# Kernel tuning notes

Hardware: AMD Instinct MI355X
Metric: run time of the kernel (lower is better)

Reference implementation:

```python
import jax, jax.numpy as jnp
import numpy as np

B, N, K, C_IN, M, C_OUT = 2, 20000, 16, 128, 9, 128


def setup_inputs() -> dict:
    key = jax.random.key(0)
    k1, k2, k3, k4, k5, k6 = jax.random.split(key, 6)
    x = jax.random.normal(k1, (B, N, C_IN), dtype=jnp.float32)
    # 0 == "no neighbor" (maps to the prepended zero row); valid ids are 1..N
    adj = jax.random.randint(k2, (N, K), 0, N, dtype=jnp.int32)
    W = jax.random.uniform(k3, (M, C_OUT, C_IN), jnp.float32, -0.05, 0.05)
    b = jax.random.uniform(k4, (C_OUT,), jnp.float32, -0.05, 0.05)
    u = jax.random.uniform(k5, (M, C_IN), jnp.float32, -0.05, 0.05)
    c = jax.random.uniform(k6, (M,), jnp.float32, -0.05, 0.05)
    return {"x": x, "adj": adj, "W": W, "b": b, "u": u, "c": c}


def reference(x, adj, W, b, u, c):
    Bb, Nn, Cin = x.shape
    # prepend zero row so adj==0 gathers zeros (padding neighbor)
    xp = jnp.concatenate([jnp.zeros((Bb, 1, Cin), x.dtype), x], axis=1)
    patches = xp[:, adj]                      # [B, N, K, C] neighbor features
    # pseudo-coordinate differences -> soft assignment over M kernels
    diff = x[:, :, None, :] - patches          # [B, N, K, C]
    logits = jnp.einsum('bnkc,mc->bnkm', diff, u) + c
    q = jax.nn.softmax(logits, axis=-1)        # softmax over M (last axis)
    # inverse neighbor count (0 where the node has no neighbors)
    deg = jnp.count_nonzero(adj, axis=1).astype(x.dtype)        # [N]
    deg_inv = jnp.where(deg > 0, 1.0 / jnp.maximum(deg, 1.0), 0.0)
    # out[b,n,o] = deg_inv[n] * sum_{k,m} q[b,n,k,m] * (W[m] @ x_nbr)[o]
    msg = jnp.einsum('bnkm,moc,bnkc->bno', q, W, patches)        # [B, N, O]
    return msg * deg_inv[None, :, None] + b
```

## Files before the change

### kernel.cpp

```cpp
#include <hip/hip_runtime.h>
#include <hip/hip_bf16.h>

#define NB 2
#define NN 20000
#define NKN 16
#define NC 128
#define NM 9
#define NO 128
#define NR (NB*NN)
#define KK 1152
#define NPB 32
#define YS 12
#define YB (NR/64)
#define SROW 2304
#define PBASE 73728u
#define SMEMB 139264

typedef short bf16x8 __attribute__((ext_vector_type(8)));
typedef short bf16x4 __attribute__((ext_vector_type(4)));
typedef float f32x4  __attribute__((ext_vector_type(4)));
typedef unsigned short u16x8 __attribute__((ext_vector_type(8)));

typedef __attribute__((address_space(1))) const void gas_void;
typedef __attribute__((address_space(3))) void las_void;

union frg8 { bf16x4 h[2]; bf16x8 v; };

__device__ inline unsigned short bfb(float f) {
    union { __hip_bfloat16 b; unsigned short u; } t;
    t.b = __float2bfloat16(f);
    return t.u;
}

__global__ __launch_bounds__(256) void prep_kernel(const float* __restrict__ x,
                                                   const float* __restrict__ u,
                                                   const float* __restrict__ W,
                                                   float* __restrict__ y,
                                                   __hip_bfloat16* __restrict__ xb,
                                                   __hip_bfloat16* __restrict__ Wg,
                                                   int use_xb) {
    int tid = threadIdx.x;
    if (blockIdx.x < YB) {
        int wave = tid >> 6, lane = tid & 63;
        int lr = lane & 15, quad = lane >> 4;
        int node0 = blockIdx.x * 64 + wave * 16;
        long xbase = (long)(node0 + lr) * NC;

        bf16x8 afr[4];
        #pragma unroll
        for (int kc = 0; kc < 4; kc++) {
            const float* px = x + xbase + kc * 32 + quad * 8;
            float4 a0 = *(const float4*)px;
            float4 a1 = *(const float4*)(px + 4);
            union { bf16x8 v; unsigned short s[8]; __hip_bfloat16 h[8]; } af;
            af.h[0] = __float2bfloat16(a0.x); af.h[1] = __float2bfloat16(a0.y);
            af.h[2] = __float2bfloat16(a0.z); af.h[3] = __float2bfloat16(a0.w);
            af.h[4] = __float2bfloat16(a1.x); af.h[5] = __float2bfloat16(a1.y);
            af.h[6] = __float2bfloat16(a1.z); af.h[7] = __float2bfloat16(a1.w);
            afr[kc] = af.v;
            if (use_xb)
                *(u16x8*)((unsigned short*)xb + xbase + kc * 32 + quad * 8) =
                    *(u16x8*)&af.v;
        }
        int cs = (lr < NM) ? lr : 0;
        float fz = (lr < NM) ? 1.f : 0.f;
        f32x4 acc = (f32x4){0.f, 0.f, 0.f, 0.f};
        #pragma unroll
        for (int kc = 0; kc < 4; kc++) {
            const float* pu = u + cs * NC + kc * 32 + quad * 8;
            float4 b0 = *(const float4*)pu;
            float4 b1 = *(const float4*)(pu + 4);
            union { bf16x8 v; __hip_bfloat16 h[8]; } bf;
            bf.h[0] = __float2bfloat16(b0.x * fz); bf.h[1] = __float2bfloat16(b0.y * fz);
            bf.h[2] = __float2bfloat16(b0.z * fz); bf.h[3] = __float2bfloat16(b0.w * fz);
            bf.h[4] = __float2bfloat16(b1.x * fz); bf.h[5] = __float2bfloat16(b1.y * fz);
            bf.h[6] = __float2bfloat16(b1.z * fz); bf.h[7] = __float2bfloat16(b1.w * fz);
            acc = __builtin_amdgcn_mfma_f32_16x16x32_bf16(afr[kc], bf.v, acc, 0, 0, 0);
        }
        if (lr < NM) {
            #pragma unroll
            for (int r = 0; r < 4; r++)
                y[(long)(node0 + quad * 4 + r) * YS + lr] = acc[r];
        }
    } else {
        int t = (blockIdx.x - YB) * 256 + tid;
        int kk = t >> 7;
        int o = t & 127;
        int ctt = kk / 144;
        int rem = kk - ctt * 144;
        int m = rem >> 4;
        int ci = rem & 15;
        float v = W[m * 16384 + o * 128 + ctt * 16 + ci];
        Wg[((kk >> 5) * 128 + o) * 32 + (kk & 31)] = __float2bfloat16(v);
    }
}

template<bool BF16G>
__global__ __launch_bounds__(1024, 4) void fused_kernel(const float* __restrict__ x,
                                                        const __hip_bfloat16* __restrict__ xb,
                                                        const int* __restrict__ adj,
                                                        const float* __restrict__ y,
                                                        const float* __restrict__ cv,
                                                        const __hip_bfloat16* __restrict__ Wg,
                                                        const float* __restrict__ bv,
                                                        float* __restrict__ out) {
    __shared__ __align__(16) char smem[SMEMB];

    int tid = threadIdx.x;
    int lane = tid & 63, wv = tid >> 6;
    int lr = lane & 15, quad = lane >> 4;
    int node0 = blockIdx.x * NPB;
    int b = node0 / NN;
    int n0 = node0 - b * NN;

    bool sm = (lane < 32);
    int lnode = wv * 2 + (quad & 1);
    int a = 0;
    if (sm) a = adj[(n0 + lnode) * NKN + lr];
    int rowint = b * NN + ((a > 0) ? a - 1 : 0);

    float4 yn0 = {0,0,0,0}, yn1 = {0,0,0,0}, ya0 = {0,0,0,0}, ya1 = {0,0,0,0};
    float yn8 = 0.f, ya8 = 0.f;
    if (sm) {
        const float* yn = y + (long)(node0 + lnode) * YS;
        const float* ya = y + (long)rowint * YS;
        yn0 = *(const float4*)yn;  yn1 = *(const float4*)(yn + 4);  yn8 = yn[8];
        ya0 = *(const float4*)ya;  ya1 = *(const float4*)(ya + 4);  ya8 = ya[8];
    }

    unsigned long long mk = __ballot(a > 0);
    int d = (int)__popcll((mk >> (quad * 16)) & 0xFFFFull);
    float di = (d > 0) ? 1.f / (float)d : 0.f;

    int pos = lane & 31;
    int e   = ((pos >> 3) << 2) | ((pos >> 1) & 3);
    int hh  = pos & 1;
    int ctl = lane >> 5;
    int rowA = __shfl(rowint, e);
    int rowB = __shfl(rowint, 16 + e);

    unsigned wboff = PBASE + (unsigned)(wv * 4096);
    unsigned sb = (unsigned)(uintptr_t)&smem[0];
    unsigned wba = sb + wboff;

    if (sm) {
        float sel = (a > 0) ? 1.f : 0.f;
        float l[NM];
        l[0] = yn0.x - sel * ya0.x + cv[0];
        l[1] = yn0.y - sel * ya0.y + cv[1];
        l[2] = yn0.z - sel * ya0.z + cv[2];
        l[3] = yn0.w - sel * ya0.w + cv[3];
        l[4] = yn1.x - sel * ya1.x + cv[4];
        l[5] = yn1.y - sel * ya1.y + cv[5];
        l[6] = yn1.z - sel * ya1.z + cv[6];
        l[7] = yn1.w - sel * ya1.w + cv[7];
        l[8] = yn8   - sel * ya8   + cv[8];
        float mx = l[0];
        #pragma unroll
        for (int m = 1; m < NM; m++) mx = fmaxf(mx, l[m]);
        float e_[NM]; float sum = 0.f;
        #pragma unroll
        for (int m = 0; m < NM; m++) { e_[m] = expf(l[m] - mx); sum += e_[m]; }
        float qf = ((a > 0) ? (1.f / sum) : 0.f) * di;

        union { u16x8 v[2]; unsigned short s[16]; } H, L;
        #pragma unroll
        for (int m = 0; m < NM; m++) {
            float qv = e_[m] * qf;
            unsigned short hb = bfb(qv);
            union { unsigned short u; __hip_bfloat16 bb; } hv; hv.u = hb;
            H.s[m] = hb;
            L.s[m] = bfb(qv - __bfloat162float(hv.bb));
        }
        #pragma unroll
        for (int m = NM; m < 16; m++) { H.s[m] = 0; L.s[m] = 0; }

        unsigned qo = wboff + (unsigned)((quad & 1) * 1024 +
                                         (lr >> 2) * 128 + (lr & 3) * 32);
        *(u16x8*)(smem + qo)       = H.v[0];
        *(u16x8*)(smem + qo + 16)  = H.v[1];
        *(u16x8*)(smem + qo + 512) = L.v[0];
        *(u16x8*)(smem + qo + 528) = L.v[1];
    }
    asm volatile("s_waitcnt lgkmcnt(0)" ::: "memory");
    __builtin_amdgcn_sched_barrier(0);

    bf16x4 qa0, qa1, qb0, qb1;
    unsigned qra = wba + (unsigned)(quad * 256 + lr * 8);
    asm volatile("ds_read_b64_tr_b16 %0, %2 offset:0\n\t"
                 "ds_read_b64_tr_b16 %1, %2 offset:128"
                 : "=&v"(qa0), "=&v"(qa1) : "v"(qra));
    asm volatile("ds_read_b64_tr_b16 %0, %2 offset:1024\n\t"
                 "ds_read_b64_tr_b16 %1, %2 offset:1152"
                 : "=&v"(qb0), "=&v"(qb1) : "v"(qra));
    asm volatile("s_waitcnt lgkmcnt(0)" ::: "memory");
    __builtin_amdgcn_sched_barrier(0);
    frg8 fragA, fragB;
    fragA.h[0] = qa0; fragA.h[1] = qa1;
    fragB.h[0] = qb0; fragB.h[1] = qb1;

    #define ISSUE(S) {                                                          \
        long rr = (long)(((S) >> 2) ? rowB : rowA);                             \
        const __hip_bfloat16* gp = xb + rr * NC +                               \
                                   (2 * ((S) & 3) + ctl) * 16 + hh * 8;         \
        __builtin_amdgcn_global_load_lds((gas_void*)gp,                         \
            (las_void*)(smem + wboff + (unsigned)(((S) & 3) * 1024)), 16, 0, 0);\
    }

    #define PITER(S, NW) {                                                      \
        if (BF16G) {                                                            \
            asm volatile("s_waitcnt vmcnt(" #NW ")" ::: "memory");              \
            __builtin_amdgcn_sched_barrier(0);                                  \
        } else {                                                                \
            long rr_ = (long)(((S) >> 2) ? rowB : rowA);                        \
            const float* fp = x + rr_ * NC + (2 * ((S) & 3) + ctl) * 16 + hh * 8;\
            float4 f0 = *(const float4*)fp;                                     \
            float4 f1 = *(const float4*)(fp + 4);                               \
            union { u16x8 v; unsigned short s[8]; } ov;                         \
            ov.s[0] = bfb(f0.x); ov.s[1] = bfb(f0.y); ov.s[2] = bfb(f0.z);      \
            ov.s[3] = bfb(f0.w); ov.s[4] = bfb(f1.x); ov.s[5] = bfb(f1.y);      \
            ov.s[6] = bfb(f1.z); ov.s[7] = bfb(f1.w);                           \
            *(u16x8*)(smem + wboff + (unsigned)(((S) & 3) * 1024 + lane * 16))  \
                = ov.v;                                                         \
            asm volatile("s_waitcnt lgkmcnt(0)" ::: "memory");                  \
            __builtin_amdgcn_sched_barrier(0);                                  \
        }                                                                       \
        bf16x4 p0a, p0b, p1a, p1b;                                              \
        unsigned pr_ = wba + (unsigned)(((S) & 3) * 1024 +                      \
                                        (quad & 1) * 256 + lr * 8);             \
        asm volatile("ds_read_b64_tr_b16 %0, %4 offset:0\n\t"                   \
                     "ds_read_b64_tr_b16 %1, %4 offset:128\n\t"                 \
                     "ds_read_b64_tr_b16 %2, %4 offset:512\n\t"                 \
                     "ds_read_b64_tr_b16 %3, %4 offset:640"                     \
                     : "=&v"(p0a), "=&v"(p0b), "=&v"(p1a), "=&v"(p1b)           \
                     : "v"(pr_));                                               \
        asm volatile("s_waitcnt lgkmcnt(0)" ::: "memory");                      \
        __builtin_amdgcn_sched_barrier(0);                                      \
        if (BF16G && (S) < 4) { ISSUE((S) + 4) }                                \
        {                                                                       \
            int nl_ = 2 * wv + ((S) >> 2);                                      \
            unsigned swz_ = (unsigned)((nl_ & 7) << 4);                         \
            f32x4 z = (f32x4){0.f, 0.f, 0.f, 0.f};                              \
            frg8 pf; pf.h[0] = p0a; pf.h[1] = p0b;                              \
            f32x4 ac = __builtin_amdgcn_mfma_f32_16x16x32_bf16(pf.v,            \
                           ((S) >> 2) ? fragB.v : fragA.v, z, 0, 0, 0);         \
            bf16x4 sv;                                                          \
            sv[0] = (short)bfb(ac[0]); sv[1] = (short)bfb(ac[1]);               \
            sv[2] = (short)bfb(ac[2]); sv[3] = (short)bfb(ac[3]);               \
            unsigned so = ((unsigned)((2 * ((S) & 3)) * 288 + lr * 32 +         \
                                      quad * 8)) ^ swz_;                        \
            if (lr < 9) *(bf16x4*)(smem + nl_ * SROW + so) = sv;                \
            pf.h[0] = p1a; pf.h[1] = p1b;                                       \
            ac = __builtin_amdgcn_mfma_f32_16x16x32_bf16(pf.v,                  \
                     ((S) >> 2) ? fragB.v : fragA.v, z, 0, 0, 0);               \
            sv[0] = (short)bfb(ac[0]); sv[1] = (short)bfb(ac[1]);               \
            sv[2] = (short)bfb(ac[2]); sv[3] = (short)bfb(ac[3]);               \
            so = ((unsigned)((2 * ((S) & 3) + 1) * 288 + lr * 32 +              \
                             quad * 8)) ^ swz_;                                 \
            if (lr < 9) *(bf16x4*)(smem + nl_ * SROW + so) = sv;                \
        }                                                                       \
    }

    if (BF16G) {
        asm volatile("s_waitcnt vmcnt(0)" ::: "memory");
        __builtin_amdgcn_sched_barrier(0);
        ISSUE(0) ISSUE(1) ISSUE(2) ISSUE(3)
    }
    PITER(0, 3) PITER(1, 3) PITER(2, 3) PITER(3, 3)
    PITER(4, 3) PITER(5, 2) PITER(6, 1) PITER(7, 0)
    #undef PITER
    #undef ISSUE

    __syncthreads();
    __builtin_amdgcn_sched_barrier(0);

    if (wv < 8) {
        const short* wg = reinterpret_cast<const short*>(Wg);
        f32x4 acc0 = (f32x4){0.f, 0.f, 0.f, 0.f};
        f32x4 acc1 = (f32x4){0.f, 0.f, 0.f, 0.f};
        unsigned swzB = (unsigned)((lr & 7) << 4);
        #pragma unroll 9
        for (int kc = 0; kc < 36; kc++) {
            bf16x8 bfrag = *(const bf16x8*)(wg + ((kc * 128) + wv * 16 + lr) * 32
                                            + quad * 8);
            unsigned ao = ((unsigned)(kc * 64 + quad * 16)) ^ swzB;
            bf16x8 a0 = *(const bf16x8*)(smem + (unsigned)(lr * SROW) + ao);
            bf16x8 a1 = *(const bf16x8*)(smem + (unsigned)((16 + lr) * SROW) + ao);
            acc0 = __builtin_amdgcn_mfma_f32_16x16x32_bf16(a0, bfrag, acc0, 0, 0, 0);
            acc1 = __builtin_amdgcn_mfma_f32_16x16x32_bf16(a1, bfrag, acc1, 0, 0, 0);
        }

        int col = wv * 16 + lr;
        float bb = bv[col];
        int rbase = node0 + quad * 4;
        #pragma unroll
        for (int r = 0; r < 4; r++) {
            out[(long)(rbase + r) * NO + col]      = acc0[r] + bb;
            out[(long)(rbase + 16 + r) * NO + col] = acc1[r] + bb;
        }
    }
}

extern "C" void kernel_launch(void* const* d_in, const int* in_sizes, int n_in,
                              void* d_out, int out_size, void* d_ws, size_t ws_size,
                              hipStream_t stream) {
    const float* x   = (const float*)d_in[0];
    const int*   adj = (const int*)  d_in[1];
    const float* W   = (const float*)d_in[2];
    const float* bv  = (const float*)d_in[3];
    const float* u   = (const float*)d_in[4];
    const float* cv  = (const float*)d_in[5];
    float* out = (float*)d_out;

    char* ws = (char*)d_ws;
    float* y = (float*)ws;
    __hip_bfloat16* Wg = (__hip_bfloat16*)(ws + 1920000);
    __hip_bfloat16* xb = (__hip_bfloat16*)(ws + 2214912);
    bool use_xb = (ws_size >= (size_t)12454912);

    prep_kernel<<<YB + 576, 256, 0, stream>>>(x, u, W, y, use_xb ? xb : nullptr, Wg,
                                              use_xb ? 1 : 0);
    if (use_xb)
        fused_kernel<true><<<NR / NPB, 1024, 0, stream>>>(x, xb, adj, y, cv, Wg, bv, out);
    else
        fused_kernel<false><<<NR / NPB, 1024, 0, stream>>>(x, xb, adj, y, cv, Wg, bv, out);
}
```

Measured before the change: 139.4 us.

## Halve nodes per block and software-pipeline LDS transpose reads across gather stages

Cuts the block to 16 nodes and 512 threads, halving shared memory so more blocks fit per CU, and every wave now joins the final GEMM with one accumulator instead of half the waves idling. The gather loop is restructured so the transposed LDS reads for the next slot are issued before the MFMA and store of the current slot, using double-buffered fragments and finer lgkmcnt/vmcnt waits. This aims to hide LDS and global latency and raise occupancy. In exchange, each Wg fragment is now loaded by twice as many blocks, and the hand-tuned wait counts risk ordering mistakes.

```diff
diff --git a/kernel.cpp b/kernel.cpp
--- a/kernel.cpp
+++ b/kernel.cpp
@@ -9,12 +9,12 @@
 #define NO 128
 #define NR (NB*NN)
 #define KK 1152
-#define NPB 32
+#define NPB 16
 #define YS 12
 #define YB (NR/64)
 #define SROW 2304
-#define PBASE 73728u
-#define SMEMB 139264
+#define PBASE 36864u
+#define SMEMB 69632
 
 typedef short bf16x8 __attribute__((ext_vector_type(8)));
 typedef short bf16x4 __attribute__((ext_vector_type(4)));
@@ -96,14 +96,14 @@
 }
 
 template<bool BF16G>
-__global__ __launch_bounds__(1024, 4) void fused_kernel(const float* __restrict__ x,
-                                                        const __hip_bfloat16* __restrict__ xb,
-                                                        const int* __restrict__ adj,
-                                                        const float* __restrict__ y,
-                                                        const float* __restrict__ cv,
-                                                        const __hip_bfloat16* __restrict__ Wg,
-                                                        const float* __restrict__ bv,
-                                                        float* __restrict__ out) {
+__global__ __launch_bounds__(512, 4) void fused_kernel(const float* __restrict__ x,
+                                                       const __hip_bfloat16* __restrict__ xb,
+                                                       const int* __restrict__ adj,
+                                                       const float* __restrict__ y,
+                                                       const float* __restrict__ cv,
+                                                       const __hip_bfloat16* __restrict__ Wg,
+                                                       const float* __restrict__ bv,
+                                                       float* __restrict__ out) {
     __shared__ __align__(16) char smem[SMEMB];
 
     int tid = threadIdx.x;
@@ -207,77 +207,101 @@
             (las_void*)(smem + wboff + (unsigned)(((S) & 3) * 1024)), 16, 0, 0);\
     }
 
-    #define PITER(S, NW) {                                                      \
-        if (BF16G) {                                                            \
-            asm volatile("s_waitcnt vmcnt(" #NW ")" ::: "memory");              \
-            __builtin_amdgcn_sched_barrier(0);                                  \
-        } else {                                                                \
-            long rr_ = (long)(((S) >> 2) ? rowB : rowA);                        \
-            const float* fp = x + rr_ * NC + (2 * ((S) & 3) + ctl) * 16 + hh * 8;\
-            float4 f0 = *(const float4*)fp;                                     \
-            float4 f1 = *(const float4*)(fp + 4);                               \
-            union { u16x8 v; unsigned short s[8]; } ov;                         \
-            ov.s[0] = bfb(f0.x); ov.s[1] = bfb(f0.y); ov.s[2] = bfb(f0.z);      \
-            ov.s[3] = bfb(f0.w); ov.s[4] = bfb(f1.x); ov.s[5] = bfb(f1.y);      \
-            ov.s[6] = bfb(f1.z); ov.s[7] = bfb(f1.w);                           \
-            *(u16x8*)(smem + wboff + (unsigned)(((S) & 3) * 1024 + lane * 16))  \
-                = ov.v;                                                         \
-            asm volatile("s_waitcnt lgkmcnt(0)" ::: "memory");                  \
-            __builtin_amdgcn_sched_barrier(0);                                  \
-        }                                                                       \
-        bf16x4 p0a, p0b, p1a, p1b;                                              \
-        unsigned pr_ = wba + (unsigned)(((S) & 3) * 1024 +                      \
-                                        (quad & 1) * 256 + lr * 8);             \
+    #define TRREAD(D0, D1, D2, D3, SLOT) {                                      \
+        unsigned pr_ = wba + (unsigned)((SLOT) * 1024 + (quad & 1) * 256 +      \
+                                        lr * 8);                                \
         asm volatile("ds_read_b64_tr_b16 %0, %4 offset:0\n\t"                   \
                      "ds_read_b64_tr_b16 %1, %4 offset:128\n\t"                 \
                      "ds_read_b64_tr_b16 %2, %4 offset:512\n\t"                 \
                      "ds_read_b64_tr_b16 %3, %4 offset:640"                     \
-                     : "=&v"(p0a), "=&v"(p0b), "=&v"(p1a), "=&v"(p1b)           \
+                     : "=&v"(D0), "=&v"(D1), "=&v"(D2), "=&v"(D3)               \
                      : "v"(pr_));                                               \
-        asm volatile("s_waitcnt lgkmcnt(0)" ::: "memory");                      \
-        __builtin_amdgcn_sched_barrier(0);                                      \
-        if (BF16G && (S) < 4) { ISSUE((S) + 4) }                                \
-        {                                                                       \
-            int nl_ = 2 * wv + ((S) >> 2);                                      \
-            unsigned swz_ = (unsigned)((nl_ & 7) << 4);                         \
-            f32x4 z = (f32x4){0.f, 0.f, 0.f, 0.f};                              \
-            frg8 pf; pf.h[0] = p0a; pf.h[1] = p0b;                              \
-            f32x4 ac = __builtin_amdgcn_mfma_f32_16x16x32_bf16(pf.v,            \
-                           ((S) >> 2) ? fragB.v : fragA.v, z, 0, 0, 0);         \
-            bf16x4 sv;                                                          \
-            sv[0] = (short)bfb(ac[0]); sv[1] = (short)bfb(ac[1]);               \
-            sv[2] = (short)bfb(ac[2]); sv[3] = (short)bfb(ac[3]);               \
-            unsigned so = ((unsigned)((2 * ((S) & 3)) * 288 + lr * 32 +         \
-                                      quad * 8)) ^ swz_;                        \
-            if (lr < 9) *(bf16x4*)(smem + nl_ * SROW + so) = sv;                \
-            pf.h[0] = p1a; pf.h[1] = p1b;                                       \
-            ac = __builtin_amdgcn_mfma_f32_16x16x32_bf16(pf.v,                  \
-                     ((S) >> 2) ? fragB.v : fragA.v, z, 0, 0, 0);               \
-            sv[0] = (short)bfb(ac[0]); sv[1] = (short)bfb(ac[1]);               \
-            sv[2] = (short)bfb(ac[2]); sv[3] = (short)bfb(ac[3]);               \
-            so = ((unsigned)((2 * ((S) & 3) + 1) * 288 + lr * 32 +              \
-                             quad * 8)) ^ swz_;                                 \
-            if (lr < 9) *(bf16x4*)(smem + nl_ * SROW + so) = sv;                \
-        }                                                                       \
+    }
+
+    #define MFMA_STORE(S, F0, F1, F2, F3) {                                     \
+        int nl_ = 2 * wv + ((S) >> 2);                                          \
+        unsigned swz_ = (unsigned)((nl_ & 7) << 4);                             \
+        f32x4 z = (f32x4){0.f, 0.f, 0.f, 0.f};                                  \
+        frg8 pf; pf.h[0] = F0; pf.h[1] = F1;                                    \
+        f32x4 ac = __builtin_amdgcn_mfma_f32_16x16x32_bf16(pf.v,                \
+                       ((S) >> 2) ? fragB.v : fragA.v, z, 0, 0, 0);             \
+        bf16x4 sv;                                                              \
+        sv[0] = (short)bfb(ac[0]); sv[1] = (short)bfb(ac[1]);                   \
+        sv[2] = (short)bfb(ac[2]); sv[3] = (short)bfb(ac[3]);                   \
+        unsigned so = ((unsigned)((2 * ((S) & 3)) * 288 + lr * 32 +             \
+                                  quad * 8)) ^ swz_;                            \
+        if (lr < 9) *(bf16x4*)(smem + nl_ * SROW + so) = sv;                    \
+        pf.h[0] = F2; pf.h[1] = F3;                                             \
+        ac = __builtin_amdgcn_mfma_f32_16x16x32_bf16(pf.v,                      \
+                 ((S) >> 2) ? fragB.v : fragA.v, z, 0, 0, 0);                   \
+        sv[0] = (short)bfb(ac[0]); sv[1] = (short)bfb(ac[1]);                   \
+        sv[2] = (short)bfb(ac[2]); sv[3] = (short)bfb(ac[3]);                   \
+        so = ((unsigned)((2 * ((S) & 3) + 1) * 288 + lr * 32 +                  \
+                         quad * 8)) ^ swz_;                                     \
+        if (lr < 9) *(bf16x4*)(smem + nl_ * SROW + so) = sv;                    \
     }
 
     if (BF16G) {
+        #define ITER(S, LKS, VWS, C0, C1, C2, C3, N0, N1, N2, N3, DOV) {        \
+            asm volatile("s_waitcnt lgkmcnt(" LKS ")" ::: "memory");            \
+            __builtin_amdgcn_sched_barrier(0);                                  \
+            if ((S) < 4) { ISSUE((S) + 4) }                                     \
+            if (DOV) {                                                          \
+                asm volatile("s_waitcnt vmcnt(" VWS ")" ::: "memory");          \
+                __builtin_amdgcn_sched_barrier(0);                              \
+                TRREAD(N0, N1, N2, N3, ((S) + 1) & 3)                           \
+            }                                                                   \
+            MFMA_STORE(S, C0, C1, C2, C3)                                       \
+        }
+
         asm volatile("s_waitcnt vmcnt(0)" ::: "memory");
         __builtin_amdgcn_sched_barrier(0);
         ISSUE(0) ISSUE(1) ISSUE(2) ISSUE(3)
-    }
-    PITER(0, 3) PITER(1, 3) PITER(2, 3) PITER(3, 3)
-    PITER(4, 3) PITER(5, 2) PITER(6, 1) PITER(7, 0)
-    #undef PITER
+        asm volatile("s_waitcnt vmcnt(3)" ::: "memory");
+        __builtin_amdgcn_sched_barrier(0);
+        bf16x4 cf0, cf1, cf2, cf3, nf0, nf1, nf2, nf3;
+        TRREAD(cf0, cf1, cf2, cf3, 0)
+
+        ITER(0, "0", "3", cf0, cf1, cf2, cf3, nf0, nf1, nf2, nf3, 1)
+        ITER(1, "2", "3", nf0, nf1, nf2, nf3, cf0, cf1, cf2, cf3, 1)
+        ITER(2, "2", "3", cf0, cf1, cf2, cf3, nf0, nf1, nf2, nf3, 1)
+        ITER(3, "2", "3", nf0, nf1, nf2, nf3, cf0, cf1, cf2, cf3, 1)
+        ITER(4, "2", "2", cf0, cf1, cf2, cf3, nf0, nf1, nf2, nf3, 1)
+        ITER(5, "2", "1", nf0, nf1, nf2, nf3, cf0, cf1, cf2, cf3, 1)
+        ITER(6, "2", "0", cf0, cf1, cf2, cf3, nf0, nf1, nf2, nf3, 1)
+        ITER(7, "2", "0", nf0, nf1, nf2, nf3, cf0, cf1, cf2, cf3, 0)
+        #undef ITER
+    } else {
+        #pragma unroll
+        for (int S = 0; S < 8; ++S) {
+            long rr_ = (long)((S >= 4) ? rowB : rowA);
+            const float* fp = x + rr_ * NC + (2 * (S & 3) + ctl) * 16 + hh * 8;
+            float4 f0 = *(const float4*)fp;
+            float4 f1 = *(const float4*)(fp + 4);
+            union { u16x8 v; unsigned short s[8]; } ov;
+            ov.s[0] = bfb(f0.x); ov.s[1] = bfb(f0.y); ov.s[2] = bfb(f0.z);
+            ov.s[3] = bfb(f0.w); ov.s[4] = bfb(f1.x); ov.s[5] = bfb(f1.y);
+            ov.s[6] = bfb(f1.z); ov.s[7] = bfb(f1.w);
+            *(u16x8*)(smem + wboff + (unsigned)((S & 3) * 1024 + lane * 16)) = ov.v;
+            asm volatile("s_waitcnt lgkmcnt(0)" ::: "memory");
+            __builtin_amdgcn_sched_barrier(0);
+            bf16x4 e0, e1, e2, e3;
+            TRREAD(e0, e1, e2, e3, S & 3)
+            asm volatile("s_waitcnt lgkmcnt(0)" ::: "memory");
+            __builtin_amdgcn_sched_barrier(0);
+            MFMA_STORE(S, e0, e1, e2, e3)
+        }
+    }
+    #undef MFMA_STORE
+    #undef TRREAD
     #undef ISSUE
 
     __syncthreads();
     __builtin_amdgcn_sched_barrier(0);
 
-    if (wv < 8) {
+    {
         const short* wg = reinterpret_cast<const short*>(Wg);
         f32x4 acc0 = (f32x4){0.f, 0.f, 0.f, 0.f};
-        f32x4 acc1 = (f32x4){0.f, 0.f, 0.f, 0.f};
         unsigned swzB = (unsigned)((lr & 7) << 4);
         #pragma unroll 9
         for (int kc = 0; kc < 36; kc++) {
@@ -285,19 +309,15 @@
                                             + quad * 8);
             unsigned ao = ((unsigned)(kc * 64 + quad * 16)) ^ swzB;
             bf16x8 a0 = *(const bf16x8*)(smem + (unsigned)(lr * SROW) + ao);
-            bf16x8 a1 = *(const bf16x8*)(smem + (unsigned)((16 + lr) * SROW) + ao);
             acc0 = __builtin_amdgcn_mfma_f32_16x16x32_bf16(a0, bfrag, acc0, 0, 0, 0);
-            acc1 = __builtin_amdgcn_mfma_f32_16x16x32_bf16(a1, bfrag, acc1, 0, 0, 0);
         }
 
         int col = wv * 16 + lr;
         float bb = bv[col];
         int rbase = node0 + quad * 4;
         #pragma unroll
-        for (int r = 0; r < 4; r++) {
-            out[(long)(rbase + r) * NO + col]      = acc0[r] + bb;
-            out[(long)(rbase + 16 + r) * NO + col] = acc1[r] + bb;
-        }
+        for (int r = 0; r < 4; r++)
+            out[(long)(rbase + r) * NO + col] = acc0[r] + bb;
     }
 }
 
@@ -321,7 +341,7 @@
     prep_kernel<<<YB + 576, 256, 0, stream>>>(x, u, W, y, use_xb ? xb : nullptr, Wg,
                                               use_xb ? 1 : 0);
     if (use_xb)
-        fused_kernel<true><<<NR / NPB, 1024, 0, stream>>>(x, xb, adj, y, cv, Wg, bv, out);
+        fused_kernel<true><<<NR / NPB, 512, 0, stream>>>(x, xb, adj, y, cv, Wg, bv, out);
     else
-        fused_kernel<false><<<NR / NPB, 1024, 0, stream>>>(x, xb, adj, y, cv, Wg, bv, out);
+        fused_kernel<false><<<NR / NPB, 512, 0, stream>>>(x, xb, adj, y, cv, Wg, bv, out);
 }
```

Measured after the change: 150.4 us. 1.08x slower.
